# Optimization experiments

Hardware: AMD Instinct MI355X
Metric: run time of the kernel (lower is better)

The kernel has to match this reference:

```python
import jax, jax.numpy as jnp
import numpy as np

NUM_CIRC = 5        # circles per vehicle (init kwarg)
BUFFER_DIST = 0.0   # extra separation buffer (init kwarg)


def setup_inputs() -> dict:
    key = jax.random.key(0)
    k1, k2, k3 = jax.random.split(key, 3)
    NA, T = 128, 100  # 8 scenes x 16 agents, 100 timesteps
    traj = jax.random.normal(k1, (NA, T, 4), dtype=jnp.float32)
    # spread positions over ~+-100m so collisions are sparse but present
    traj = traj.at[:, :, :2].multiply(50.0)
    # realistic vehicle attributes: length ~3-5.5m, width ~1.5-2.2m
    length = jax.random.uniform(k2, (NA,), minval=3.0, maxval=5.5, dtype=jnp.float32)
    width = jax.random.uniform(k3, (NA,), minval=1.5, maxval=2.2, dtype=jnp.float32)
    veh_att = jnp.stack([length, width], axis=1)
    ptr = jnp.arange(9) * 16  # 8 scenes of 16 agents each
    return {"traj": traj, "veh_att": veh_att, "ptr": ptr}


def _forward(traj, veh_att, ptr):
    NA, T, _ = traj.shape
    C = NUM_CIRC
    veh_rad = veh_att[:, 1] * 0.5
    half_len = veh_att[:, 0] * 0.5
    cent_min = -half_len + veh_rad
    cent_max = half_len - veh_rad
    # per-vehicle circle centers along the length axis (local frame): NA x C
    frac = jnp.linspace(0.0, 1.0, C, dtype=traj.dtype)
    cent_x = cent_min[:, None] + (cent_max - cent_min)[:, None] * frac[None, :]
    # transform2frame(traj, centroids, inverse=True): rotate local (cx, 0) by the
    # (normalized) heading and translate by position -> world = pos + cx * h_unit
    pos = traj[:, :, :2]                                   # NA,T,2
    h = traj[:, :, 2:4]
    h = h / jnp.linalg.norm(h, axis=-1, keepdims=True)     # unit heading
    world_cent = pos[:, :, None, :] + cent_x[:, None, :, None] * h[:, :, None, :]  # NA,T,C,2
    world_cent = jnp.transpose(world_cent, (1, 0, 2, 3))   # T,NA,C,2
    # pairwise circle distances: T,NA,NA,C,C (matches torch.cdist over circle dims)
    diff = world_cent[:, :, None, :, None, :] - world_cent[:, None, :, None, :, :]
    sq = jnp.sum(diff * diff, axis=-1)
    pos_sq = sq > 0
    dists = jnp.where(pos_sq, jnp.sqrt(jnp.where(pos_sq, sq, 1.0)), 0.0)
    min_pair_dists = jnp.min(dists.reshape(T, NA, NA, C * C), axis=-1)  # T,NA,NA
    penalty_dists = veh_rad[:, None] + veh_rad[None, :] + BUFFER_DIST   # NA,NA
    # valid pairs: same scene (via ptr) and off-diagonal
    scene_id = jnp.searchsorted(ptr[1:], jnp.arange(NA), side="right")
    valid_mask = (scene_id[:, None] == scene_id[None, :]) & ~jnp.eye(NA, dtype=bool)
    colliding = (min_pair_dists <= penalty_dists[None]) & valid_mask[None]
    penalties = jnp.where(colliding, 1.0 - min_pair_dists / penalty_dists[None],
                          jnp.zeros((), dtype=traj.dtype))
    graph_sizes = ptr[1:] - ptr[:-1]
    num_pairs = jnp.sum(graph_sizes * graph_sizes - graph_sizes)
    # NOTE: torch gathers penalties[valid_mask] (dynamic shape); we return the
    # dense T,NA,NA tensor which is zero exactly at invalid entries, so any
    # reduction (sum/mean over valid pairs) matches.
    return penalties, num_pairs


def reference(traj, veh_att, ptr):
    return _forward(traj, veh_att, ptr)
```

## Files before the change

kernel.cpp:

```cpp
#include <hip/hip_runtime.h>

#define NAG 128
#define TT  100
#define NC  5
#define PB_PER_T 16
#define PAIRS_PER_BLOCK 1024
#define PPT 4

__global__ __launch_bounds__(256) void vehcoll_kernel(
    const float* __restrict__ traj,
    const float* __restrict__ veh_att,
    const int*   __restrict__ ptr,
    float* __restrict__ out,
    int n_ptr)
{
    __shared__ float s_cx[NC][NAG];
    __shared__ float s_cy[NC][NAG];
    __shared__ float s_rad[NAG];
    __shared__ int   s_scene[NAG];

    const int t   = blockIdx.x >> 4;
    const int pb  = blockIdx.x & 15;
    const int tid = threadIdx.x;

    if (tid < NAG) {
        const int a = tid;
        float4 tr = *(const float4*)(traj + ((size_t)a * TT + t) * 4);
        float len = veh_att[a * 2 + 0];
        float wid = veh_att[a * 2 + 1];
        float rad  = 0.5f * wid;
        float cmin = rad - 0.5f * len;
        float step = 0.25f * (len - wid);
        float inv  = 1.0f / sqrtf(tr.z * tr.z + tr.w * tr.w);
        float hx = tr.z * inv, hy = tr.w * inv;
        #pragma unroll
        for (int c = 0; c < NC; ++c) {
            float cx = cmin + step * (float)c;
            s_cx[c][a] = tr.x + cx * hx;
            s_cy[c][a] = tr.y + cx * hy;
        }
        s_rad[a] = rad;
        int sc = 0;
        for (int k = 1; k < n_ptr; ++k) sc += (ptr[k] <= a) ? 1 : 0;
        s_scene[a] = sc;
    }
    __syncthreads();

    const int p0 = pb * PAIRS_PER_BLOCK + tid * PPT;
    const int i  = p0 >> 7;
    const int j0 = p0 & 127;

    float pen[PPT] = {0.f, 0.f, 0.f, 0.f};
    const int sci = s_scene[i];
    if (sci >= s_scene[j0] && sci <= s_scene[j0 + PPT - 1]) {
        float ix[NC], iy[NC];
        #pragma unroll
        for (int c = 0; c < NC; ++c) { ix[c] = s_cx[c][i]; iy[c] = s_cy[c][i]; }
        const float ri = s_rad[i];
        #pragma unroll
        for (int q = 0; q < PPT; ++q) {
            const int j = j0 + q;
            float minsq = 3.4e38f;
            #pragma unroll
            for (int ci = 0; ci < NC; ++ci) {
                const float jxc = 0.0f; (void)jxc;
                #pragma unroll
                for (int cj = 0; cj < NC; ++cj) {
                    float dx = ix[ci] - s_cx[cj][j];
                    float dy = iy[ci] - s_cy[cj][j];
                    minsq = fminf(minsq, dx * dx + dy * dy);
                }
            }
            float d  = sqrtf(minsq);
            float pd = ri + s_rad[j];
            bool valid = (i != j) && (sci == s_scene[j]);
            pen[q] = (valid && d <= pd) ? 1.0f - d / pd : 0.0f;
        }
    }
    *(float4*)(out + (size_t)t * NAG * NAG + p0) =
        make_float4(pen[0], pen[1], pen[2], pen[3]);

    if (blockIdx.x == 0 && tid == 0) {
        int np = 0;
        for (int k = 0; k + 1 < n_ptr; ++k) {
            int g = ptr[k + 1] - ptr[k];
            np += g * g - g;
        }
        out[(size_t)TT * NAG * NAG] = (float)np;
    }
}

extern "C" void kernel_launch(void* const* d_in, const int* in_sizes, int n_in,
                              void* d_out, int out_size, void* d_ws, size_t ws_size,
                              hipStream_t stream) {
    const float* traj    = (const float*)d_in[0];
    const float* veh_att = (const float*)d_in[1];
    const int*   ptr     = (const int*)d_in[2];
    float*       out     = (float*)d_out;
    const int n_ptr = in_sizes[2];

    dim3 grid(TT * PB_PER_T);
    dim3 block(256);
    hipLaunchKernelGGL(vehcoll_kernel, grid, block, 0, stream,
                       traj, veh_att, ptr, out, n_ptr);
}
```

Measured before the change: 66.33 us.

## Tile per timestep and scene, computing only intra-scene pairs

The grid becomes (timestep, scene). Each block zero-fills its scene's rows of the output, builds circle centres only for that scene's agents, and evaluates only the g×g pairs inside the scene. This drops the per-agent scene-id search and the blocks that mostly did scene checks on cross-scene pairs. In exchange, outputs are written with scalar scattered stores instead of aligned float4 stores. Parallelism now depends on how many agents each scene has.

```diff
diff --git a/kernel.cpp b/kernel.cpp
--- a/kernel.cpp
+++ b/kernel.cpp
@@ -3,9 +3,6 @@
 #define NAG 128
 #define TT  100
 #define NC  5
-#define PB_PER_T 16
-#define PAIRS_PER_BLOCK 1024
-#define PPT 4
 
 __global__ __launch_bounds__(256) void vehcoll_kernel(
     const float* __restrict__ traj,
@@ -17,14 +14,36 @@
     __shared__ float s_cx[NC][NAG];
     __shared__ float s_cy[NC][NAG];
     __shared__ float s_rad[NAG];
-    __shared__ int   s_scene[NAG];
 
-    const int t   = blockIdx.x >> 4;
-    const int pb  = blockIdx.x & 15;
+    const int t   = blockIdx.x;
+    const int s   = blockIdx.y;
     const int tid = threadIdx.x;
 
-    if (tid < NAG) {
-        const int a = tid;
+    if (t == 0 && s == 0 && tid == 0) {
+        int np = 0;
+        for (int k = 0; k + 1 < n_ptr; ++k) {
+            int gg = ptr[k + 1] - ptr[k];
+            np += gg * gg - gg;
+        }
+        out[(size_t)TT * NAG * NAG] = (float)np;
+    }
+
+    int a0 = (s == 0) ? 0 : ptr[s];
+    int a1 = (s == n_ptr - 1) ? NAG : ptr[s + 1];
+    a0 = min(max(a0, 0), NAG);
+    a1 = min(max(a1, a0), NAG);
+    const int g = a1 - a0;
+    if (g <= 0) return;
+
+    float* rowbase = out + (size_t)t * NAG * NAG + (size_t)a0 * NAG;
+
+    const int nvec = g * (NAG / 4);
+    float4 z = make_float4(0.f, 0.f, 0.f, 0.f);
+    for (int u = tid; u < nvec; u += 256)
+        ((float4*)rowbase)[u] = z;
+
+    if (tid < g) {
+        const int a = a0 + tid;
         float4 tr = *(const float4*)(traj + ((size_t)a * TT + t) * 4);
         float len = veh_att[a * 2 + 0];
         float wid = veh_att[a * 2 + 1];
@@ -36,57 +55,40 @@
         #pragma unroll
         for (int c = 0; c < NC; ++c) {
             float cx = cmin + step * (float)c;
-            s_cx[c][a] = tr.x + cx * hx;
-            s_cy[c][a] = tr.y + cx * hy;
+            s_cx[c][tid] = tr.x + cx * hx;
+            s_cy[c][tid] = tr.y + cx * hy;
         }
-        s_rad[a] = rad;
-        int sc = 0;
-        for (int k = 1; k < n_ptr; ++k) sc += (ptr[k] <= a) ? 1 : 0;
-        s_scene[a] = sc;
+        s_rad[tid] = rad;
     }
     __syncthreads();
 
-    const int p0 = pb * PAIRS_PER_BLOCK + tid * PPT;
-    const int i  = p0 >> 7;
-    const int j0 = p0 & 127;
+    const int npair = g * g;
+    for (int p = tid; p < npair; p += 256) {
+        const int li = p / g;
+        const int lj = p - li * g;
+        if (li == lj) continue;
 
-    float pen[PPT] = {0.f, 0.f, 0.f, 0.f};
-    const int sci = s_scene[i];
-    if (sci >= s_scene[j0] && sci <= s_scene[j0 + PPT - 1]) {
-        float ix[NC], iy[NC];
+        float ixr[NC], iyr[NC], jxr[NC], jyr[NC];
         #pragma unroll
-        for (int c = 0; c < NC; ++c) { ix[c] = s_cx[c][i]; iy[c] = s_cy[c][i]; }
-        const float ri = s_rad[i];
+        for (int c = 0; c < NC; ++c) {
+            ixr[c] = s_cx[c][li];  iyr[c] = s_cy[c][li];
+            jxr[c] = s_cx[c][lj];  jyr[c] = s_cy[c][lj];
+        }
+
+        float minsq = 3.4e38f;
         #pragma unroll
-        for (int q = 0; q < PPT; ++q) {
-            const int j = j0 + q;
-            float minsq = 3.4e38f;
+        for (int ci = 0; ci < NC; ++ci) {
             #pragma unroll
-            for (int ci = 0; ci < NC; ++ci) {
-                const float jxc = 0.0f; (void)jxc;
-                #pragma unroll
-                for (int cj = 0; cj < NC; ++cj) {
-                    float dx = ix[ci] - s_cx[cj][j];
-                    float dy = iy[ci] - s_cy[cj][j];
-                    minsq = fminf(minsq, dx * dx + dy * dy);
-                }
+            for (int cj = 0; cj < NC; ++cj) {
+                float dx = ixr[ci] - jxr[cj];
+                float dy = iyr[ci] - jyr[cj];
+                minsq = fminf(minsq, dx * dx + dy * dy);
             }
-            float d  = sqrtf(minsq);
-            float pd = ri + s_rad[j];
-            bool valid = (i != j) && (sci == s_scene[j]);
-            pen[q] = (valid && d <= pd) ? 1.0f - d / pd : 0.0f;
         }
-    }
-    *(float4*)(out + (size_t)t * NAG * NAG + p0) =
-        make_float4(pen[0], pen[1], pen[2], pen[3]);
-
-    if (blockIdx.x == 0 && tid == 0) {
-        int np = 0;
-        for (int k = 0; k + 1 < n_ptr; ++k) {
-            int g = ptr[k + 1] - ptr[k];
-            np += g * g - g;
-        }
-        out[(size_t)TT * NAG * NAG] = (float)np;
+        float d  = sqrtf(minsq);
+        float pd = s_rad[li] + s_rad[lj];
+        float pen = (d <= pd) ? 1.0f - d / pd : 0.0f;
+        rowbase[li * NAG + a0 + lj] = pen;
     }
 }
 
@@ -99,7 +101,7 @@
     float*       out     = (float*)d_out;
     const int n_ptr = in_sizes[2];
 
-    dim3 grid(TT * PB_PER_T);
+    dim3 grid(TT, n_ptr > 0 ? n_ptr : 1);
     dim3 block(256);
     hipLaunchKernelGGL(vehcoll_kernel, grid, block, 0, stream,
                        traj, veh_att, ptr, out, n_ptr);
```

Measured after the change: 61.27 us. 7.6% less time.
